# Optimization experiments

Measured on AMD Instinct MI355X. Metric: run time of the kernel, lower is better.

Reference implementation:

```python
import jax, jax.numpy as jnp
import numpy as np

H = 512

def setup_inputs() -> dict:
    key = jax.random.key(0)
    ks = jax.random.split(key, 24)
    B, Tv, Tt = 64, 512, 64
    def W(k):
        return jax.random.normal(k, (H, H), dtype=jnp.float32) * 0.01
    def v(k):
        return jax.random.normal(k, (H,), dtype=jnp.float32) * 0.01
    return {
        "h": jax.random.normal(ks[0], (B, H), dtype=jnp.float32),
        "hidden_frames": jax.random.normal(ks[1], (B, Tv, H), dtype=jnp.float32),
        "hidden_text": jax.random.normal(ks[2], (B, Tt, H), dtype=jnp.float32),
        "Wav": W(ks[3]), "Wat": W(ks[4]), "Uav": W(ks[5]), "Uat": W(ks[6]),
        "Vav": v(ks[7]), "Vat": v(ks[8]),
        "bav": jnp.zeros((H,), jnp.float32), "bat": jnp.zeros((H,), jnp.float32),
        "Whh": W(ks[9]), "bh": jnp.zeros((H,), jnp.float32),
        "Wve": jax.random.normal(ks[10], (H, H), dtype=jnp.float32) * 0.02,
        "bve": jnp.zeros((H,), jnp.float32),
        "Wqe": jax.random.normal(ks[11], (H, H), dtype=jnp.float32) * 0.02,
        "bqe": jnp.zeros((H,), jnp.float32),
        "Wb": W(ks[12]), "Vbv": W(ks[13]), "Vbt": W(ks[14]),
        "bbv": jnp.zeros((H,), jnp.float32), "bbt": jnp.zeros((H,), jnp.float32),
        "wb": v(ks[15]),
    }

def reference(h, hidden_frames, hidden_text, Wav, Wat, Uav, Uat, Vav, Vat,
              bav, bat, Whh, bh, Wve, bve, Wqe, bqe, Wb, Vbv, Vbt, bbv, bbt, wb):
    # Additive (Bahdanau) attention over frames, conditioned on h
    Uhv = (h @ Uav)[:, None, :]                                   # [B,1,H]
    Uht = (h @ Uat)[:, None, :]
    score_v = jnp.tanh(hidden_frames @ Wav + Uhv + bav) @ Vav     # [B,Tv]
    score_t = jnp.tanh(hidden_text @ Wat + Uht + bat) @ Vat       # [B,Tt]
    av = jax.nn.softmax(score_v, axis=1)
    at = jax.nn.softmax(score_t, axis=1)
    hv_sum = jnp.einsum('bt,bth->bh', av, hidden_frames)          # [B,H]
    ht_sum = jnp.einsum('bt,bth->bh', at, hidden_text)
    hv_sum2 = hv_sum @ Wve.T + bve                                # Linear encoders
    ht_sum2 = ht_sum @ Wqe.T + bqe
    # Gating between the two streams (blp is None -> concat path)
    Wbs = h @ Wb
    mt1 = ht_sum @ Vbt + bbt + Wbs
    mv1 = hv_sum @ Vbv + bbv + Wbs
    mtv = jnp.tanh(jnp.concatenate([mv1, mt1], axis=0))           # [2B,H]
    beta = jax.nn.softmax(mtv @ wb, axis=0)                       # [2B]
    out = jnp.tanh(h @ Whh + beta[0] * hv_sum2 + beta[1] * ht_sum2 + bh)
    return out                                                     # [B,H]
```

## Files before the change

### kernel.cpp

```cpp
#include <hip/hip_runtime.h>
#include <stdint.h>
#include <stddef.h>

#define H  512
#define BB 64
#define TV 512
#define TT 64

typedef short s8v __attribute__((ext_vector_type(8)));
typedef float f4v __attribute__((ext_vector_type(4)));


__device__ inline unsigned short f2bf(float f) {
  unsigned int u = __float_as_uint(f);
  u = (u + 0x7fffu + ((u >> 16) & 1u)) >> 16;
  return (unsigned short)u;
}

__device__ inline unsigned int pk2bf(float lo, float hi) {
  unsigned int a = __float_as_uint(lo);
  a = (a + 0x7fffu + ((a >> 16) & 1u)) >> 16;
  unsigned int b = __float_as_uint(hi);
  b = (b + 0x7fffu + ((b >> 16) & 1u)) & 0xffff0000u;
  return a | b;
}

__device__ inline float fast_tanh(float x) {
  x = fminf(15.f, fmaxf(-15.f, x));
  float e = __expf(2.f * x);
  return (e - 1.f) * __builtin_amdgcn_rcpf(e + 1.f);
}

__device__ inline void gld16(const unsigned short* g, unsigned short* l) {
  __builtin_amdgcn_global_load_lds(
      (const __attribute__((address_space(1))) unsigned int*)g,
      (__attribute__((address_space(3))) unsigned int*)l, 16, 0, 0);
}

__global__ void k_conv(const float* __restrict__ F, const float* __restrict__ Txt,
                       const float* __restrict__ h,
                       unsigned short* __restrict__ Fb, unsigned short* __restrict__ Tb,
                       unsigned short* __restrict__ hb) {
  const size_t NF = (size_t)BB * TV * H;
  const size_t NT = (size_t)BB * TT * H;
  const size_t NH = (size_t)BB * H;
  size_t i = ((size_t)blockIdx.x * 256 + threadIdx.x) * 8;
  const float* src; unsigned short* dst;
  if (i < NF) { src = F + i; dst = Fb + i; }
  else if (i < NF + NT) { size_t j = i - NF; src = Txt + j; dst = Tb + j; }
  else { size_t j = i - NF - NT; if (j >= NH) return; src = h + j; dst = hb + j; }
  float4 f0 = *(const float4*)src;
  float4 f1 = *(const float4*)(src + 4);
  uint4 p;
  p.x = pk2bf(f0.x, f0.y); p.y = pk2bf(f0.z, f0.w);
  p.z = pk2bf(f1.x, f1.y); p.w = pk2bf(f1.z, f1.w);
  *(uint4*)dst = p;
}

__global__ void k_conv2(const float* __restrict__ src, unsigned short* __restrict__ dst) {
  size_t i = ((size_t)blockIdx.x * 256 + threadIdx.x) * 8;
  float4 f0 = *(const float4*)(src + i);
  float4 f1 = *(const float4*)(src + i + 4);
  uint4 p;
  p.x = pk2bf(f0.x, f0.y); p.y = pk2bf(f0.z, f0.w);
  p.z = pk2bf(f1.x, f1.y); p.w = pk2bf(f1.z, f1.w);
  *(uint4*)(dst + i) = p;
}

__global__ void k_prep_w(const float* __restrict__ Wav, const float* __restrict__ Wat,
                         const float* __restrict__ Uav, const float* __restrict__ Uat,
                         const float* __restrict__ Wb,  const float* __restrict__ Whh,
                         const float* __restrict__ Wve, const float* __restrict__ Wqe,
                         const float* __restrict__ Vbv, const float* __restrict__ Vbt,
                         unsigned short* __restrict__ Wbf) {
  __shared__ float tile[64][65];
  const int z = blockIdx.z;
  const float* src =
      (z == 0) ? Wav : (z == 1) ? Wat : (z == 2) ? Uav : (z == 3) ? Uat :
      (z == 4) ? Wb  : (z == 5) ? Whh : (z == 6) ? Wve : (z == 7) ? Wqe :
      (z == 8) ? Vbv : Vbt;
  unsigned short* dst = Wbf + (size_t)z * H * H;
  const int k0 = blockIdx.x * 64, j0 = blockIdx.y * 64;
  const int tid = threadIdx.x;
  if (z == 6 || z == 7) {
    for (int i = 0; i < 16; ++i) {
      int e = tid + i * 256; int r = e >> 6, c = e & 63;
      dst[(size_t)(k0 + r) * H + j0 + c] = f2bf(src[(size_t)(k0 + r) * H + j0 + c]);
    }
    return;
  }
  for (int i = 0; i < 16; ++i) {
    int e = tid + i * 256; int r = e >> 6, c = e & 63;
    tile[r][c] = src[(size_t)(k0 + r) * H + j0 + c];
  }
  __syncthreads();
  for (int i = 0; i < 16; ++i) {
    int e = tid + i * 256; int r = e >> 6, c = e & 63;
    dst[(size_t)(j0 + r) * H + k0 + c] = f2bf(tile[c][r]);
  }
}

__global__ __launch_bounds__(256)
void k_gemm64(const unsigned short* __restrict__ A0, const unsigned short* __restrict__ A1,
              const unsigned short* __restrict__ Bt, float* __restrict__ C,
              const float* __restrict__ bias0, const float* __restrict__ bias1,
              int aMode) {
  __shared__ unsigned short As[64 * 32];
  __shared__ unsigned short Bs[64 * 32];
  const int tid = threadIdx.x;
  const int n0 = blockIdx.x * 64;
  const int seg = blockIdx.y;
  const unsigned short* A = (aMode && (seg & 1)) ? A1 : A0;
  const unsigned short* B = Bt + (size_t)seg * H * H;

  const int r = tid >> 2, c = (tid & 3) * 8;
  const unsigned short* Ag = A + (size_t)r * H + c;
  const unsigned short* Bg = B + (size_t)(n0 + r) * H + c;
  unsigned short* Al = &As[tid * 8];
  unsigned short* Bl = &Bs[tid * 8];

  const int wv = tid >> 6, ln = tid & 63;
  const int quad = ln >> 4, l16 = ln & 15;
  const int wm = (wv >> 1) * 32, wn = (wv & 1) * 32;

  f4v acc[2][2] = {};
  for (int k0 = 0; k0 < H; k0 += 32) {
    __syncthreads();
    gld16(Ag + k0, Al);
    gld16(Bg + k0, Bl);
    __syncthreads();
    s8v afr[2], bfr[2];
#pragma unroll
    for (int mi = 0; mi < 2; ++mi)
      afr[mi] = *(const s8v*)&As[(wm + mi * 16 + l16) * 32 + quad * 8];
#pragma unroll
    for (int ni = 0; ni < 2; ++ni)
      bfr[ni] = *(const s8v*)&Bs[(wn + ni * 16 + l16) * 32 + quad * 8];
#pragma unroll
    for (int mi = 0; mi < 2; ++mi)
#pragma unroll
      for (int ni = 0; ni < 2; ++ni)
        acc[mi][ni] = __builtin_amdgcn_mfma_f32_16x16x32_bf16(afr[mi], bfr[ni], acc[mi][ni], 0, 0, 0);
  }

  const float* bias = (seg == 0) ? bias0 : (seg == 1) ? bias1 : nullptr;
  float* Cs = C + (size_t)seg * BB * H;
#pragma unroll
  for (int mi = 0; mi < 2; ++mi)
#pragma unroll
    for (int ni = 0; ni < 2; ++ni)
#pragma unroll
      for (int rr = 0; rr < 4; ++rr) {
        const int row = wm + mi * 16 + quad * 4 + rr;
        const int j = n0 + wn + ni * 16 + l16;
        float v = acc[mi][ni][rr];
        if (bias) v += bias[j];
        Cs[(size_t)row * H + j] = v;
      }
}

template <int LOGT>
__global__ __launch_bounds__(256)
void k_score(const unsigned short* __restrict__ A, const unsigned short* __restrict__ Bt,
             const float* __restrict__ uvw, const float* __restrict__ V,
             float* __restrict__ score) {
  constexpr int T = 1 << LOGT;
  __shared__ unsigned short As[128 * 32];
  __shared__ unsigned short Bs[128 * 32];
  const int tid = threadIdx.x;
  const int m0 = blockIdx.x * 128;
  const int n0 = blockIdx.y * 128;
  const int wv = tid >> 6, ln = tid & 63;
  const int quad = ln >> 4, l16 = ln & 15;
  const int wm = (wv >> 1) * 64, wn = (wv & 1) * 64;

  const int s0 = wv * 128 + ln;
  const int s1 = s0 + 64;
  const int r0 = s0 >> 2, c0 = (s0 & 3) * 8;
  const int r1 = s1 >> 2, c1 = (s1 & 3) * 8;

  const unsigned short* Ag0 = A + (size_t)(m0 + r0) * H + c0;
  const unsigned short* Ag1 = A + (size_t)(m0 + r1) * H + c1;
  const unsigned short* Bg0 = Bt + (size_t)(n0 + r0) * H + c0;
  const unsigned short* Bg1 = Bt + (size_t)(n0 + r1) * H + c1;
  unsigned short* Al0 = &As[s0 * 8];
  unsigned short* Al1 = &As[s1 * 8];
  unsigned short* Bl0 = &Bs[s0 * 8];
  unsigned short* Bl1 = &Bs[s1 * 8];

  f4v acc[4][4] = {};

  for (int k0 = 0; k0 < H; k0 += 32) {
    __syncthreads();
    gld16(Ag0 + k0, Al0);
    gld16(Ag1 + k0, Al1);
    gld16(Bg0 + k0, Bl0);
    gld16(Bg1 + k0, Bl1);
    __syncthreads();
    s8v afr[4], bfr[4];
#pragma unroll
    for (int mi = 0; mi < 4; ++mi)
      afr[mi] = *(const s8v*)&As[(wm + mi * 16 + l16) * 32 + quad * 8];
#pragma unroll
    for (int ni = 0; ni < 4; ++ni)
      bfr[ni] = *(const s8v*)&Bs[(wn + ni * 16 + l16) * 32 + quad * 8];
#pragma unroll
    for (int mi = 0; mi < 4; ++mi)
#pragma unroll
      for (int ni = 0; ni < 4; ++ni)
        acc[mi][ni] = __builtin_amdgcn_mfma_f32_16x16x32_bf16(afr[mi], bfr[ni], acc[mi][ni], 0, 0, 0);
  }

  int jj[4]; float vv[4];
#pragma unroll
  for (int ni = 0; ni < 4; ++ni) {
    jj[ni] = n0 + wn + ni * 16 + l16;
    vv[ni] = V[jj[ni]];
  }
#pragma unroll
  for (int mi = 0; mi < 4; ++mi) {
    const int mrow0 = m0 + wm + mi * 16;
    const int bidx = mrow0 >> LOGT;
    const float* up = uvw + (size_t)bidx * H;
    float uu[4];
#pragma unroll
    for (int ni = 0; ni < 4; ++ni) uu[ni] = up[jj[ni]];
#pragma unroll
    for (int r = 0; r < 4; ++r) {
      float sum = 0.f;
#pragma unroll
      for (int ni = 0; ni < 4; ++ni)
        sum += fast_tanh(acc[mi][ni][r] + uu[ni]) * vv[ni];
      sum += __shfl_xor(sum, 1);
      sum += __shfl_xor(sum, 2);
      sum += __shfl_xor(sum, 4);
      sum += __shfl_xor(sum, 8);
      if (l16 == 0) {
        const int mrow = mrow0 + quad * 4 + r;
        atomicAdd(&score[(size_t)bidx * T + (mrow & (T - 1))], sum);
      }
    }
  }
}

__global__ void k_softmax(float* __restrict__ score_v, float* __restrict__ score_t) {
  __shared__ float red[4];
  const int i = blockIdx.x, tid = threadIdx.x;
  const bool fr = i < BB;
  float* sc = fr ? (score_v + i * TV) : (score_t + (i - BB) * TT);
  const int T = fr ? TV : TT;
  float v0 = (tid < T) ? sc[tid] : -1e30f;
  float v1 = fr ? sc[tid + 256] : -1e30f;
  float mx = fmaxf(v0, v1);
  for (int d = 32; d; d >>= 1) mx = fmaxf(mx, __shfl_xor(mx, d));
  if ((tid & 63) == 0) red[tid >> 6] = mx;
  __syncthreads();
  mx = fmaxf(fmaxf(red[0], red[1]), fmaxf(red[2], red[3]));
  __syncthreads();
  float e0 = (tid < T) ? __expf(v0 - mx) : 0.f;
  float e1 = fr ? __expf(v1 - mx) : 0.f;
  float se = e0 + e1;
  for (int d = 32; d; d >>= 1) se += __shfl_xor(se, d);
  if ((tid & 63) == 0) red[tid >> 6] = se;
  __syncthreads();
  const float inv = 1.f / (red[0] + red[1] + red[2] + red[3]);
  if (tid < T) sc[tid] = e0 * inv;
  if (fr) sc[tid + 256] = e1 * inv;
}

__global__ void k_wsum(const unsigned short* __restrict__ Fb, const unsigned short* __restrict__ Tb,
                       const float* __restrict__ aw_v, const float* __restrict__ aw_t,
                       float* __restrict__ hv_sum, float* __restrict__ ht_sum) {
  __shared__ float w[64];
  const int b = blockIdx.x, ch = blockIdx.y, tid = threadIdx.x;
  const bool fr = ch < 8;
  const unsigned short* X = fr ? (Fb + ((size_t)b * TV + ch * 64) * H)
                               : (Tb + (size_t)b * TT * H);
  const float* ww = fr ? (aw_v + b * TV + ch * 64) : (aw_t + b * TT);
  float* out = fr ? (hv_sum + b * H) : (ht_sum + b * H);
  if (tid < 64) w[tid] = ww[tid];
  __syncthreads();
  const int j = tid * 2;
  float a0 = 0.f, a1 = 0.f;
  for (int t = 0; t < 64; ++t) {
    unsigned u = *(const unsigned*)(X + (size_t)t * H + j);
    float wt = w[t];
    a0 += wt * __uint_as_float(u << 16);
    a1 += wt * __uint_as_float(u & 0xffff0000u);
  }
  atomicAdd(&out[j], a0);
  atomicAdd(&out[j + 1], a1);
}

__global__ void k_gate(const float* __restrict__ CB, const float* __restrict__ wbs,
                       const float* __restrict__ bbv, const float* __restrict__ bbt,
                       const float* __restrict__ wb, float* __restrict__ sArr) {
  __shared__ float red[4];
  const int i = blockIdx.x, tid = threadIdx.x;
  const bool fr = i < BB;
  const int b = fr ? i : i - BB;
  const float* m1 = CB + (size_t)(fr ? 2 : 3) * BB * H + (size_t)b * H;
  const float* b2 = fr ? bbv : bbt;
  float sp = 0.f;
#pragma unroll
  for (int jj = 0; jj < 2; ++jj) {
    int j = tid + jj * 256;
    float g = m1[j] + wbs[(size_t)b * H + j] + b2[j];
    sp += fast_tanh(g) * wb[j];
  }
  for (int d = 32; d; d >>= 1) sp += __shfl_xor(sp, d);
  if ((tid & 63) == 0) red[tid >> 6] = sp;
  __syncthreads();
  if (tid == 0) sArr[i] = red[0] + red[1] + red[2] + red[3];
}

__global__ void k_final2(const float* __restrict__ sArr, const float* __restrict__ hwhh,
                         const float* __restrict__ bh,
                         const float* __restrict__ hv2, const float* __restrict__ ht2,
                         const float* __restrict__ bve, const float* __restrict__ bqe,
                         float* __restrict__ out) {
  __shared__ float red[4];
  const int b = blockIdx.x, tid = threadIdx.x;
  float v = (tid < 2 * BB) ? sArr[tid] : -1e30f;
  float mx = v;
  for (int d = 32; d; d >>= 1) mx = fmaxf(mx, __shfl_xor(mx, d));
  if ((tid & 63) == 0) red[tid >> 6] = mx;
  __syncthreads();
  mx = fmaxf(fmaxf(red[0], red[1]), fmaxf(red[2], red[3]));
  __syncthreads();
  float e = (tid < 2 * BB) ? __expf(v - mx) : 0.f;
  for (int d = 32; d; d >>= 1) e += __shfl_xor(e, d);
  if ((tid & 63) == 0) red[tid >> 6] = e;
  __syncthreads();
  const float Z = red[0] + red[1] + red[2] + red[3];
  const float beta0 = __expf(sArr[0] - mx) / Z;
  const float beta1 = __expf(sArr[1] - mx) / Z;
#pragma unroll
  for (int jj = 0; jj < 2; ++jj) {
    int j = tid + jj * 256;
    float x = hwhh[(size_t)b * H + j] + bh[j]
            + beta0 * (hv2[(size_t)b * H + j] + bve[j])
            + beta1 * (ht2[(size_t)b * H + j] + bqe[j]);
    out[(size_t)b * H + j] = fast_tanh(x);
  }
}


extern "C" void kernel_launch(void* const* d_in, const int* in_sizes, int n_in,
                              void* d_out, int out_size, void* d_ws, size_t ws_size,
                              hipStream_t stream) {
  const float* h    = (const float*)d_in[0];
  const float* F    = (const float*)d_in[1];
  const float* Txt  = (const float*)d_in[2];
  const float* Wav  = (const float*)d_in[3];
  const float* Wat  = (const float*)d_in[4];
  const float* Uav  = (const float*)d_in[5];
  const float* Uat  = (const float*)d_in[6];
  const float* Vav  = (const float*)d_in[7];
  const float* Vat  = (const float*)d_in[8];
  const float* bav  = (const float*)d_in[9];
  const float* bat  = (const float*)d_in[10];
  const float* Whh  = (const float*)d_in[11];
  const float* bh   = (const float*)d_in[12];
  const float* Wve  = (const float*)d_in[13];
  const float* bve  = (const float*)d_in[14];
  const float* Wqe  = (const float*)d_in[15];
  const float* bqe  = (const float*)d_in[16];
  const float* Wb   = (const float*)d_in[17];
  const float* Vbv  = (const float*)d_in[18];
  const float* Vbt  = (const float*)d_in[19];
  const float* bbv  = (const float*)d_in[20];
  const float* bbt  = (const float*)d_in[21];
  const float* wb   = (const float*)d_in[22];
  float* out = (float*)d_out;

  char* ws = (char*)d_ws;
  size_t off = 0;
  auto alloc = [&](size_t bytes) -> void* {
    void* p = ws + off;
    off += (bytes + 255) & ~(size_t)255;
    return p;
  };
  float* score_v = (float*)alloc((size_t)BB * TV * 4);
  float* score_t = (float*)alloc((size_t)BB * TT * 4);
  float* hv_sum  = (float*)alloc((size_t)BB * H * 4);
  float* ht_sum  = (float*)alloc((size_t)BB * H * 4);
  unsigned short* Wbf = (unsigned short*)alloc((size_t)10 * H * H * 2);
  unsigned short* Fb  = (unsigned short*)alloc((size_t)BB * TV * H * 2);
  unsigned short* Tb  = (unsigned short*)alloc((size_t)BB * TT * H * 2);
  unsigned short* hb  = (unsigned short*)alloc((size_t)BB * H * 2);
  unsigned short* hvhtb = (unsigned short*)alloc((size_t)2 * BB * H * 2);
  float* CA   = (float*)alloc((size_t)4 * BB * H * 4);
  float* CB   = (float*)alloc((size_t)4 * BB * H * 4);
  float* sArr = (float*)alloc((size_t)2 * BB * 4);

  float* uv   = CA;
  float* ut   = CA + (size_t)BB * H;
  float* wbs  = CA + (size_t)2 * BB * H;
  float* hwhh = CA + (size_t)3 * BB * H;

  hipMemsetAsync(score_v, 0, (size_t)(BB * TV + BB * TT + 2 * BB * H) * 4, stream);

  const size_t NTOT = (size_t)BB * (TV + TT + 1) * H;
  k_conv<<<dim3(NTOT / 8 / 256), 256, 0, stream>>>(F, Txt, h, Fb, Tb, hb);
  k_prep_w<<<dim3(8, 8, 10), 256, 0, stream>>>(Wav, Wat, Uav, Uat, Wb, Whh,
                                               Wve, Wqe, Vbv, Vbt, Wbf);
  k_gemm64<<<dim3(8, 4), 256, 0, stream>>>(hb, nullptr, Wbf + (size_t)2 * H * H,
                                           CA, bav, bat, 0);
  k_score<9><<<dim3(BB * TV / 128, 4), 256, 0, stream>>>(Fb, Wbf, uv, Vav, score_v);
  k_score<6><<<dim3(BB * TT / 128, 4), 256, 0, stream>>>(Tb, Wbf + (size_t)H * H, ut, Vat, score_t);
  k_softmax<<<128, 256, 0, stream>>>(score_v, score_t);
  k_wsum<<<dim3(64, 9), 256, 0, stream>>>(Fb, Tb, score_v, score_t, hv_sum, ht_sum);
  k_conv2<<<dim3(2 * BB * H / 8 / 256), 256, 0, stream>>>(hv_sum, hvhtb);
  k_gemm64<<<dim3(8, 4), 256, 0, stream>>>(hvhtb, hvhtb + (size_t)BB * H,
                                           Wbf + (size_t)6 * H * H, CB,
                                           nullptr, nullptr, 1);
  k_gate<<<128, 256, 0, stream>>>(CB, wbs, bbv, bbt, wb, sArr);
  k_final2<<<64, 256, 0, stream>>>(sArr, hwhh, bh, CB, CB + (size_t)BB * H,
                                   bve, bqe, out);
}
```

Before: 234.8 us.

## Fuse prep, score, softmax and conversion kernels to cut launch count

Merges the input conversion and weight transpose into one prep kernel, and merges the frame and text score GEMMs into a single launch. Softmax is folded into the weighted-sum kernel, which recomputes it per chunk. The bf16 conversion of hv/ht sums moves into the second GEMM's A-tile load. The aim is to remove four kernel launches and their inter-kernel gaps. In exchange, each wsum block redoes the softmax reduction, and the A operand of gemmB is now a fp32 register load instead of an async LDS load.

```diff
diff --git a/kernel.cpp b/kernel.cpp
--- a/kernel.cpp
+++ b/kernel.cpp
@@ -37,51 +37,39 @@
       (__attribute__((address_space(3))) unsigned int*)l, 16, 0, 0);
 }
 
-__global__ void k_conv(const float* __restrict__ F, const float* __restrict__ Txt,
+__global__ void k_prep(const float* __restrict__ F, const float* __restrict__ Txt,
                        const float* __restrict__ h,
+                       const float* __restrict__ Wav, const float* __restrict__ Wat,
+                       const float* __restrict__ Uav, const float* __restrict__ Uat,
+                       const float* __restrict__ Wb,  const float* __restrict__ Whh,
+                       const float* __restrict__ Wve, const float* __restrict__ Wqe,
+                       const float* __restrict__ Vbv, const float* __restrict__ Vbt,
                        unsigned short* __restrict__ Fb, unsigned short* __restrict__ Tb,
-                       unsigned short* __restrict__ hb) {
-  const size_t NF = (size_t)BB * TV * H;
-  const size_t NT = (size_t)BB * TT * H;
-  const size_t NH = (size_t)BB * H;
-  size_t i = ((size_t)blockIdx.x * 256 + threadIdx.x) * 8;
-  const float* src; unsigned short* dst;
-  if (i < NF) { src = F + i; dst = Fb + i; }
-  else if (i < NF + NT) { size_t j = i - NF; src = Txt + j; dst = Tb + j; }
-  else { size_t j = i - NF - NT; if (j >= NH) return; src = h + j; dst = hb + j; }
-  float4 f0 = *(const float4*)src;
-  float4 f1 = *(const float4*)(src + 4);
-  uint4 p;
-  p.x = pk2bf(f0.x, f0.y); p.y = pk2bf(f0.z, f0.w);
-  p.z = pk2bf(f1.x, f1.y); p.w = pk2bf(f1.z, f1.w);
-  *(uint4*)dst = p;
-}
-
-__global__ void k_conv2(const float* __restrict__ src, unsigned short* __restrict__ dst) {
-  size_t i = ((size_t)blockIdx.x * 256 + threadIdx.x) * 8;
-  float4 f0 = *(const float4*)(src + i);
-  float4 f1 = *(const float4*)(src + i + 4);
-  uint4 p;
-  p.x = pk2bf(f0.x, f0.y); p.y = pk2bf(f0.z, f0.w);
-  p.z = pk2bf(f1.x, f1.y); p.w = pk2bf(f1.z, f1.w);
-  *(uint4*)(dst + i) = p;
-}
-
-__global__ void k_prep_w(const float* __restrict__ Wav, const float* __restrict__ Wat,
-                         const float* __restrict__ Uav, const float* __restrict__ Uat,
-                         const float* __restrict__ Wb,  const float* __restrict__ Whh,
-                         const float* __restrict__ Wve, const float* __restrict__ Wqe,
-                         const float* __restrict__ Vbv, const float* __restrict__ Vbt,
-                         unsigned short* __restrict__ Wbf) {
+                       unsigned short* __restrict__ hb, unsigned short* __restrict__ Wbf) {
   __shared__ float tile[64][65];
-  const int z = blockIdx.z;
+  const int bx = blockIdx.x, tid = threadIdx.x;
+  if (bx < 9232) {
+    const float* src; unsigned short* dst; size_t base;
+    if (bx < 8192)      { base = (size_t)bx * 2048;          src = F;   dst = Fb; }
+    else if (bx < 9216) { base = (size_t)(bx - 8192) * 2048; src = Txt; dst = Tb; }
+    else                { base = (size_t)(bx - 9216) * 2048; src = h;   dst = hb; }
+    size_t i = base + (size_t)tid * 8;
+    float4 f0 = *(const float4*)(src + i);
+    float4 f1 = *(const float4*)(src + i + 4);
+    uint4 p;
+    p.x = pk2bf(f0.x, f0.y); p.y = pk2bf(f0.z, f0.w);
+    p.z = pk2bf(f1.x, f1.y); p.w = pk2bf(f1.z, f1.w);
+    *(uint4*)(dst + i) = p;
+    return;
+  }
+  const int z = (bx - 9232) >> 6;
+  const int t = (bx - 9232) & 63;
+  const int k0 = (t >> 3) * 64, j0 = (t & 7) * 64;
   const float* src =
       (z == 0) ? Wav : (z == 1) ? Wat : (z == 2) ? Uav : (z == 3) ? Uat :
       (z == 4) ? Wb  : (z == 5) ? Whh : (z == 6) ? Wve : (z == 7) ? Wqe :
       (z == 8) ? Vbv : Vbt;
   unsigned short* dst = Wbf + (size_t)z * H * H;
-  const int k0 = blockIdx.x * 64, j0 = blockIdx.y * 64;
-  const int tid = threadIdx.x;
   if (z == 6 || z == 7) {
     for (int i = 0; i < 16; ++i) {
       int e = tid + i * 256; int r = e >> 6, c = e & 63;
@@ -101,20 +89,18 @@
 }
 
 __global__ __launch_bounds__(256)
-void k_gemm64(const unsigned short* __restrict__ A0, const unsigned short* __restrict__ A1,
-              const unsigned short* __restrict__ Bt, float* __restrict__ C,
-              const float* __restrict__ bias0, const float* __restrict__ bias1,
-              int aMode) {
+void k_gemmA(const unsigned short* __restrict__ A0, const unsigned short* __restrict__ Bt,
+             float* __restrict__ C,
+             const float* __restrict__ bias0, const float* __restrict__ bias1) {
   __shared__ unsigned short As[64 * 32];
   __shared__ unsigned short Bs[64 * 32];
   const int tid = threadIdx.x;
   const int n0 = blockIdx.x * 64;
   const int seg = blockIdx.y;
-  const unsigned short* A = (aMode && (seg & 1)) ? A1 : A0;
   const unsigned short* B = Bt + (size_t)seg * H * H;
 
   const int r = tid >> 2, c = (tid & 3) * 8;
-  const unsigned short* Ag = A + (size_t)r * H + c;
+  const unsigned short* Ag = A0 + (size_t)r * H + c;
   const unsigned short* Bg = B + (size_t)(n0 + r) * H + c;
   unsigned short* Al = &As[tid * 8];
   unsigned short* Bl = &Bs[tid * 8];
@@ -159,17 +145,26 @@
       }
 }
 
-template <int LOGT>
 __global__ __launch_bounds__(256)
-void k_score(const unsigned short* __restrict__ A, const unsigned short* __restrict__ Bt,
-             const float* __restrict__ uvw, const float* __restrict__ V,
-             float* __restrict__ score) {
-  constexpr int T = 1 << LOGT;
+void k_score(const unsigned short* __restrict__ Fb, const unsigned short* __restrict__ Tb,
+             const unsigned short* __restrict__ Wbf,
+             const float* __restrict__ uv, const float* __restrict__ ut,
+             const float* __restrict__ Vav, const float* __restrict__ Vat,
+             float* __restrict__ score_v, float* __restrict__ score_t) {
   __shared__ unsigned short As[128 * 32];
   __shared__ unsigned short Bs[128 * 32];
   const int tid = threadIdx.x;
-  const int m0 = blockIdx.x * 128;
+  const int bx = blockIdx.x;
+  const bool fr = bx < 256;
+  const int m0 = (fr ? bx : bx - 256) * 128;
   const int n0 = blockIdx.y * 128;
+  const int logT = fr ? 9 : 6;
+  const unsigned short* A = fr ? Fb : Tb;
+  const unsigned short* Bt = fr ? Wbf : (Wbf + (size_t)H * H);
+  const float* uvw = fr ? uv : ut;
+  const float* V = fr ? Vav : Vat;
+  float* score = fr ? score_v : score_t;
+
   const int wv = tid >> 6, ln = tid & 63;
   const int quad = ln >> 4, l16 = ln & 15;
   const int wm = (wv >> 1) * 64, wn = (wv & 1) * 64;
@@ -217,10 +212,11 @@
     jj[ni] = n0 + wn + ni * 16 + l16;
     vv[ni] = V[jj[ni]];
   }
+  const int tmask = (1 << logT) - 1;
 #pragma unroll
   for (int mi = 0; mi < 4; ++mi) {
     const int mrow0 = m0 + wm + mi * 16;
-    const int bidx = mrow0 >> LOGT;
+    const int bidx = mrow0 >> logT;
     const float* up = uvw + (size_t)bidx * H;
     float uu[4];
 #pragma unroll
@@ -237,18 +233,22 @@
       sum += __shfl_xor(sum, 8);
       if (l16 == 0) {
         const int mrow = mrow0 + quad * 4 + r;
-        atomicAdd(&score[(size_t)bidx * T + (mrow & (T - 1))], sum);
+        atomicAdd(&score[((size_t)bidx << logT) + (mrow & tmask)], sum);
       }
     }
   }
 }
 
-__global__ void k_softmax(float* __restrict__ score_v, float* __restrict__ score_t) {
+__global__ void k_wsum(const unsigned short* __restrict__ Fb, const unsigned short* __restrict__ Tb,
+                       const float* __restrict__ score_v, const float* __restrict__ score_t,
+                       float* __restrict__ hv_sum, float* __restrict__ ht_sum) {
+  __shared__ float w[64];
   __shared__ float red[4];
-  const int i = blockIdx.x, tid = threadIdx.x;
-  const bool fr = i < BB;
-  float* sc = fr ? (score_v + i * TV) : (score_t + (i - BB) * TT);
+  const int b = blockIdx.x, ch = blockIdx.y, tid = threadIdx.x;
+  const bool fr = ch < 8;
+  const float* sc = fr ? (score_v + b * TV) : (score_t + b * TT);
   const int T = fr ? TV : TT;
+
   float v0 = (tid < T) ? sc[tid] : -1e30f;
   float v1 = fr ? sc[tid + 256] : -1e30f;
   float mx = fmaxf(v0, v1);
@@ -264,22 +264,13 @@
   if ((tid & 63) == 0) red[tid >> 6] = se;
   __syncthreads();
   const float inv = 1.f / (red[0] + red[1] + red[2] + red[3]);
-  if (tid < T) sc[tid] = e0 * inv;
-  if (fr) sc[tid + 256] = e1 * inv;
-}
-
-__global__ void k_wsum(const unsigned short* __restrict__ Fb, const unsigned short* __restrict__ Tb,
-                       const float* __restrict__ aw_v, const float* __restrict__ aw_t,
-                       float* __restrict__ hv_sum, float* __restrict__ ht_sum) {
-  __shared__ float w[64];
-  const int b = blockIdx.x, ch = blockIdx.y, tid = threadIdx.x;
-  const bool fr = ch < 8;
-  const unsigned short* X = fr ? (Fb + ((size_t)b * TV + ch * 64) * H)
+  const int t0 = fr ? ch * 64 : 0;
+  if (tid < 64) w[tid] = __expf(sc[t0 + tid] - mx) * inv;
+  __syncthreads();
+
+  const unsigned short* X = fr ? (Fb + ((size_t)b * TV + t0) * H)
                                : (Tb + (size_t)b * TT * H);
-  const float* ww = fr ? (aw_v + b * TV + ch * 64) : (aw_t + b * TT);
   float* out = fr ? (hv_sum + b * H) : (ht_sum + b * H);
-  if (tid < 64) w[tid] = ww[tid];
-  __syncthreads();
   const int j = tid * 2;
   float a0 = 0.f, a1 = 0.f;
   for (int t = 0; t < 64; ++t) {
@@ -290,6 +281,64 @@
   }
   atomicAdd(&out[j], a0);
   atomicAdd(&out[j + 1], a1);
+}
+
+__global__ __launch_bounds__(256)
+void k_gemmB(const float* __restrict__ Afp, const unsigned short* __restrict__ Bt,
+             float* __restrict__ C) {
+  __shared__ unsigned short As[64 * 32];
+  __shared__ unsigned short Bs[64 * 32];
+  const int tid = threadIdx.x;
+  const int n0 = blockIdx.x * 64;
+  const int seg = blockIdx.y;
+  const float* A = Afp + (size_t)((seg & 1) ? BB * H : 0);
+  const unsigned short* B = Bt + (size_t)seg * H * H;
+
+  const int r = tid >> 2, c = (tid & 3) * 8;
+  const float* Ag = A + (size_t)r * H + c;
+  const unsigned short* Bg = B + (size_t)(n0 + r) * H + c;
+  unsigned short* Bl = &Bs[tid * 8];
+
+  const int wv = tid >> 6, ln = tid & 63;
+  const int quad = ln >> 4, l16 = ln & 15;
+  const int wm = (wv >> 1) * 32, wn = (wv & 1) * 32;
+
+  f4v acc[2][2] = {};
+  for (int k0 = 0; k0 < H; k0 += 32) {
+    __syncthreads();
+    float4 f0 = *(const float4*)(Ag + k0);
+    float4 f1 = *(const float4*)(Ag + k0 + 4);
+    uint4 p;
+    p.x = pk2bf(f0.x, f0.y); p.y = pk2bf(f0.z, f0.w);
+    p.z = pk2bf(f1.x, f1.y); p.w = pk2bf(f1.z, f1.w);
+    *(uint4*)&As[tid * 8] = p;
+    gld16(Bg + k0, Bl);
+    __syncthreads();
+    s8v afr[2], bfr[2];
+#pragma unroll
+    for (int mi = 0; mi < 2; ++mi)
+      afr[mi] = *(const s8v*)&As[(wm + mi * 16 + l16) * 32 + quad * 8];
+#pragma unroll
+    for (int ni = 0; ni < 2; ++ni)
+      bfr[ni] = *(const s8v*)&Bs[(wn + ni * 16 + l16) * 32 + quad * 8];
+#pragma unroll
+    for (int mi = 0; mi < 2; ++mi)
+#pragma unroll
+      for (int ni = 0; ni < 2; ++ni)
+        acc[mi][ni] = __builtin_amdgcn_mfma_f32_16x16x32_bf16(afr[mi], bfr[ni], acc[mi][ni], 0, 0, 0);
+  }
+
+  float* Cs = C + (size_t)seg * BB * H;
+#pragma unroll
+  for (int mi = 0; mi < 2; ++mi)
+#pragma unroll
+    for (int ni = 0; ni < 2; ++ni)
+#pragma unroll
+      for (int rr = 0; rr < 4; ++rr) {
+        const int row = wm + mi * 16 + quad * 4 + rr;
+        const int j = n0 + wn + ni * 16 + l16;
+        Cs[(size_t)row * H + j] = acc[mi][ni][rr];
+      }
 }
 
 __global__ void k_gate(const float* __restrict__ CB, const float* __restrict__ wbs,
@@ -389,7 +438,6 @@
   unsigned short* Fb  = (unsigned short*)alloc((size_t)BB * TV * H * 2);
   unsigned short* Tb  = (unsigned short*)alloc((size_t)BB * TT * H * 2);
   unsigned short* hb  = (unsigned short*)alloc((size_t)BB * H * 2);
-  unsigned short* hvhtb = (unsigned short*)alloc((size_t)2 * BB * H * 2);
   float* CA   = (float*)alloc((size_t)4 * BB * H * 4);
   float* CB   = (float*)alloc((size_t)4 * BB * H * 4);
   float* sArr = (float*)alloc((size_t)2 * BB * 4);
@@ -401,20 +449,13 @@
 
   hipMemsetAsync(score_v, 0, (size_t)(BB * TV + BB * TT + 2 * BB * H) * 4, stream);
 
-  const size_t NTOT = (size_t)BB * (TV + TT + 1) * H;
-  k_conv<<<dim3(NTOT / 8 / 256), 256, 0, stream>>>(F, Txt, h, Fb, Tb, hb);
-  k_prep_w<<<dim3(8, 8, 10), 256, 0, stream>>>(Wav, Wat, Uav, Uat, Wb, Whh,
-                                               Wve, Wqe, Vbv, Vbt, Wbf);
-  k_gemm64<<<dim3(8, 4), 256, 0, stream>>>(hb, nullptr, Wbf + (size_t)2 * H * H,
-                                           CA, bav, bat, 0);
-  k_score<9><<<dim3(BB * TV / 128, 4), 256, 0, stream>>>(Fb, Wbf, uv, Vav, score_v);
-  k_score<6><<<dim3(BB * TT / 128, 4), 256, 0, stream>>>(Tb, Wbf + (size_t)H * H, ut, Vat, score_t);
-  k_softmax<<<128, 256, 0, stream>>>(score_v, score_t);
+  k_prep<<<dim3(9872), 256, 0, stream>>>(F, Txt, h, Wav, Wat, Uav, Uat, Wb, Whh,
+                                         Wve, Wqe, Vbv, Vbt, Fb, Tb, hb, Wbf);
+  k_gemmA<<<dim3(8, 4), 256, 0, stream>>>(hb, Wbf + (size_t)2 * H * H, CA, bav, bat);
+  k_score<<<dim3(288, 4), 256, 0, stream>>>(Fb, Tb, Wbf, uv, ut, Vav, Vat,
+                                            score_v, score_t);
   k_wsum<<<dim3(64, 9), 256, 0, stream>>>(Fb, Tb, score_v, score_t, hv_sum, ht_sum);
-  k_conv2<<<dim3(2 * BB * H / 8 / 256), 256, 0, stream>>>(hv_sum, hvhtb);
-  k_gemm64<<<dim3(8, 4), 256, 0, stream>>>(hvhtb, hvhtb + (size_t)BB * H,
-                                           Wbf + (size_t)6 * H * H, CB,
-                                           nullptr, nullptr, 1);
+  k_gemmB<<<dim3(8, 4), 256, 0, stream>>>(hv_sum, Wbf + (size_t)6 * H * H, CB);
   k_gate<<<128, 256, 0, stream>>>(CB, wbs, bbv, bbt, wb, sArr);
   k_final2<<<64, 256, 0, stream>>>(sArr, hwhh, bh, CB, CB + (size_t)BB * H,
                                    bve, bqe, out);
```

After: 223.3 us. 1.05x faster.
